# Optimization experiments

Measured on AMD Instinct MI355X. Metric: run time of the kernel, lower is better.

## Reference

```python
import jax, jax.numpy as jnp
import numpy as np

BONUS = 10.0   # strict_maxima_bonus
EPS = 1e-07


def _quad_interp3d(x, hes_noise):
    """Faithful port of kornia-style conv_quad_interp3d (diff-mode gradients,
    replicate padding, 3x3x3 NMS, masked 3x3 solve)."""
    B, C, D, H, W = x.shape
    dt = x.dtype
    # replicate-pad by 1 in D,H,W (spatial_gradient3d pads 'replicate')
    xp = jnp.pad(x, ((0, 0), (0, 0), (1, 1), (1, 1), (1, 1)), mode='edge')
    xw_p = xp[:, :, 1:-1, 1:-1, 2:]; xw_m = xp[:, :, 1:-1, 1:-1, :-2]
    xh_p = xp[:, :, 1:-1, 2:, 1:-1]; xh_m = xp[:, :, 1:-1, :-2, 1:-1]
    xd_p = xp[:, :, 2:, 1:-1, 1:-1]; xd_m = xp[:, :, :-2, 1:-1, 1:-1]
    # first-order central differences (channel order: x=W, y=H, s=D)
    gx = 0.5 * (xw_p - xw_m)
    gy = 0.5 * (xh_p - xh_m)
    gs = 0.5 * (xd_p - xd_m)
    # second-order stencils
    dxx = xw_p - 2.0 * x + xw_m
    dyy = xh_p - 2.0 * x + xh_m
    dss = xd_p - 2.0 * x + xd_m
    dxy = 0.25 * (xp[:, :, 1:-1, :-2, :-2] - xp[:, :, 1:-1, :-2, 2:]
                  - xp[:, :, 1:-1, 2:, :-2] + xp[:, :, 1:-1, 2:, 2:])
    dys = 0.25 * (xp[:, :, :-2, :-2, 1:-1] - xp[:, :, :-2, 2:, 1:-1]
                  - xp[:, :, 2:, :-2, 1:-1] + xp[:, :, 2:, 2:, 1:-1])
    dxs = 0.25 * (xp[:, :, :-2, 1:-1, :-2] - xp[:, :, :-2, 1:-1, 2:]
                  - xp[:, :, 2:, 1:-1, :-2] + xp[:, :, 2:, 1:-1, 2:])

    N = B * C * D * H * W
    b = jnp.stack([gx, gy, gs], axis=-1).reshape(N, 3)          # (N,3)
    Hes = jnp.stack([dxx, dxy, dxs,
                     dxy, dyy, dys,
                     dxs, dys, dss], axis=-1).reshape(N, 3, 3)  # (N,3,3)
    Hes = Hes + jnp.abs(hes_noise)[None].astype(dt) * jnp.asarray(EPS, dt)

    # NMS3d: 3x3x3 max-pool (stride 1, -inf padding), mask where value == window max
    x_max = jax.lax.reduce_window(x, -jnp.inf, jax.lax.max,
                                  (1, 1, 3, 3, 3), (1, 1, 1, 1, 1), 'SAME')
    mask = (x == x_max).reshape(N)

    # masked solve: identity Hessian where not a maximum -> zero contribution
    eye3 = jnp.eye(3, dtype=dt)
    Hm = jnp.where(mask[:, None, None], Hes, eye3)
    sol = jnp.linalg.solve(Hm, b[..., None])[..., 0]            # (N,3)
    sol = jnp.where(mask[:, None], sol, jnp.zeros((), dt))

    dx = -sol
    too_big = jnp.max(jnp.abs(dx), axis=1, keepdims=True) > 0.7
    dx = jnp.where(too_big, jnp.zeros((), dt), dx)
    dy = 0.5 * jnp.sum(b * dx, axis=1)                          # 0.5 * b^T dx

    y_max = x + dy.reshape(B, C, D, H, W) + BONUS * mask.reshape(B, C, D, H, W).astype(dt)

    # flip (x,y,s) -> (s,y,x) = (d,h,w) offsets, move coord axis to dim 2
    dx_res = dx[:, ::-1].reshape(B, C, D, H, W, 3).transpose(0, 1, 5, 2, 3, 4)
    grid = jnp.stack(jnp.meshgrid(jnp.arange(D), jnp.arange(H), jnp.arange(W),
                                  indexing='ij'), axis=0).astype(dt)  # (3,D,H,W)
    coords_max = grid[None, None] + dx_res                      # (B,C,3,D,H,W)
    return coords_max, y_max


def setup_inputs() -> dict:
    key = jax.random.key(0)
    k1, k2 = jax.random.split(key)
    x = jax.random.normal(k1, (2, 1, 8, 384, 384), dtype=jnp.float32)
    hes_noise = jax.random.uniform(k2, (3, 3), dtype=jnp.float32)
    return {"x": x, "hes_noise": hes_noise}


def reference(x, hes_noise):
    return _quad_interp3d(x, hes_noise)
```

## Files before the change

kernel.cpp:

```cpp
#include <hip/hip_runtime.h>


constexpr int Dd = 8, Hh = 384, Ww = 384, BC = 2;
constexpr int HW  = Hh * Ww;
constexpr int DHW = Dd * HW;
constexpr int NVOX = BC * DHW;
constexpr int W4 = Ww / 4;

#define BONUS_ 10.0f
#define EPS_ 1e-7f

__device__ __forceinline__ void load_plane6(const float* __restrict__ pb,
                                            int ro0, int ro1, int ro2,
                                            int w4, float dst[3][6], float pmax[4]) {
    const int offm = (w4 > 0)  ? -4 : 0;
    const int offp = (w4 < 95) ?  4 : 0;
    const int ro[3] = { ro0, ro1, ro2 };
    #pragma unroll
    for (int j = 0; j < 3; j++) {
        const float* row = pb + ro[j] + (w4 << 2);
        float4 c4 = *(const float4*)(row);
        float4 m4 = *(const float4*)(row + offm);
        float4 p4 = *(const float4*)(row + offp);
        dst[j][0] = (w4 > 0)  ? m4.w : c4.x;
        dst[j][1] = c4.x; dst[j][2] = c4.y; dst[j][3] = c4.z; dst[j][4] = c4.w;
        dst[j][5] = (w4 < 95) ? p4.x : c4.w;
    }
    #pragma unroll
    for (int k = 0; k < 4; k++) {
        float m0 = fmaxf(fmaxf(dst[0][k], dst[0][k + 1]), dst[0][k + 2]);
        float m1 = fmaxf(fmaxf(dst[1][k], dst[1][k + 1]), dst[1][k + 2]);
        float m2 = fmaxf(fmaxf(dst[2][k], dst[2][k + 1]), dst[2][k + 2]);
        pmax[k] = fmaxf(fmaxf(m0, m1), m2);
    }
}

__device__ __forceinline__ void compute_store(
    const float A[3][6], const float B[3][6], const float C[3][6],
    const float pmA[4], const float pmB[4], const float pmC[4],
    const float* __restrict__ hnA,
    float* __restrict__ coords, float* __restrict__ ymax,
    int d, int h, int w0, int cbase, int ybase)
{
    float r0[4], r1[4], r2[4], ry[4];

    #pragma unroll
    for (int k = 0; k < 4; k++) {
        float c = B[1][k + 1];

        float mx = fmaxf(fmaxf(pmA[k], pmB[k]), pmC[k]);
        bool mask = (c == mx);

        float gx = 0.5f * (B[1][k + 2] - B[1][k]);
        float gy = 0.5f * (B[2][k + 1] - B[0][k + 1]);
        float gs = 0.5f * (C[1][k + 1] - A[1][k + 1]);

        float dxx = B[1][k + 2] - 2.f * c + B[1][k];
        float dyy = B[2][k + 1] - 2.f * c + B[0][k + 1];
        float dss = C[1][k + 1] - 2.f * c + A[1][k + 1];
        float dxy = 0.25f * (B[0][k] - B[0][k + 2] - B[2][k] + B[2][k + 2]);
        float dys = 0.25f * (A[0][k + 1] - A[2][k + 1] - C[0][k + 1] + C[2][k + 1]);
        float dxs = 0.25f * (A[1][k] - A[1][k + 2] - C[1][k] + C[1][k + 2]);

        float A00 = dxx + hnA[0];
        float A01 = dxy + hnA[1];
        float A02 = dxs + hnA[2];
        float A10 = dxy + hnA[3];
        float A11 = dyy + hnA[4];
        float A12 = dys + hnA[5];
        float A20 = dxs + hnA[6];
        float A21 = dys + hnA[7];
        float A22 = dss + hnA[8];
        float b0 = gx, b1 = gy, b2 = gs;

        float c00 = A11 * A22 - A12 * A21;
        float c01 = A10 * A22 - A12 * A20;
        float c02 = A10 * A21 - A11 * A20;
        float det = A00 * c00 - A01 * c01 + A02 * c02;
        float inv = 1.0f / det;

        float t0 = b1 * A22 - A12 * b2;
        float t1 = A10 * b2 - b1 * A20;
        float t2 = b1 * A21 - A11 * b2;

        float s0 = (b0 * c00 - A01 * t0 + A02 * t2) * inv;
        float s1 = (A00 * t0 - b0 * c01 + A02 * t1) * inv;
        float s2 = (-A00 * t2 - A01 * t1 + b0 * c02) * inv;

        float dxv0 = mask ? -s0 : 0.f;
        float dxv1 = mask ? -s1 : 0.f;
        float dxv2 = mask ? -s2 : 0.f;
        float amax = fmaxf(fabsf(dxv0), fmaxf(fabsf(dxv1), fabsf(dxv2)));
        if (amax > 0.7f) { dxv0 = 0.f; dxv1 = 0.f; dxv2 = 0.f; }
        float dyv = 0.5f * (gx * dxv0 + gy * dxv1 + gs * dxv2);

        r0[k] = (float)d + dxv2;
        r1[k] = (float)h + dxv1;
        r2[k] = (float)(w0 + k) + dxv0;
        ry[k] = c + dyv + (mask ? BONUS_ : 0.f);
    }

    *(float4*)(coords + cbase)           = make_float4(r0[0], r0[1], r0[2], r0[3]);
    *(float4*)(coords + cbase + DHW)     = make_float4(r1[0], r1[1], r1[2], r1[3]);
    *(float4*)(coords + cbase + 2 * DHW) = make_float4(r2[0], r2[1], r2[2], r2[3]);
    *(float4*)(ymax + ybase)             = make_float4(ry[0], ry[1], ry[2], ry[3]);
}

__global__ __launch_bounds__(256) void quad_interp3d_kernel(
    const float* __restrict__ x,
    const float* __restrict__ hn,
    float* __restrict__ out)
{
    int t = blockIdx.x * 256 + threadIdx.x;
    int w4 = t % W4;
    int r  = t / W4;
    int h  = r % Hh;
    int r2 = r / Hh;
    int dt = r2 % 4;
    int bc = r2 / 4;

    const float* xb = x + bc * DHW;
    int w0 = w4 << 2;

    int h0 = h > 0 ? h - 1 : 0;
    int h2 = h < Hh - 1 ? h + 1 : Hh - 1;
    int ro0 = h0 * Ww, ro1 = h * Ww, ro2 = h2 * Ww;

    float hnA[9];
    #pragma unroll
    for (int i = 0; i < 9; i++) hnA[i] = fabsf(hn[i]) * EPS_;

    int d0  = dt * 2;
    int pm1 = d0 > 0 ? d0 - 1 : 0;
    int pp1 = d0 + 1;
    int pp2 = d0 + 2 < Dd ? d0 + 2 : Dd - 1;

    float P0[3][6], P1[3][6], P2[3][6], P3[3][6];
    float m0[4], m1[4], m2[4], m3[4];
    load_plane6(xb + pm1 * HW, ro0, ro1, ro2, w4, P0, m0);
    load_plane6(xb + d0  * HW, ro0, ro1, ro2, w4, P1, m1);
    load_plane6(xb + pp1 * HW, ro0, ro1, ro2, w4, P2, m2);
    load_plane6(xb + pp2 * HW, ro0, ro1, ro2, w4, P3, m3);

    float* coords = out;
    float* ymax   = out + 3 * NVOX;

    int sp0 = d0 * HW + ro1 + w0;
    int cb  = bc * 3 * DHW + sp0;
    int yb  = bc * DHW + sp0;

    compute_store(P0, P1, P2, m0, m1, m2, hnA, coords, ymax, d0,     h, w0, cb,      yb);
    compute_store(P1, P2, P3, m1, m2, m3, hnA, coords, ymax, d0 + 1, h, w0, cb + HW, yb + HW);
}

extern "C" void kernel_launch(void* const* d_in, const int* in_sizes, int n_in,
                              void* d_out, int out_size, void* d_ws, size_t ws_size,
                              hipStream_t stream) {
    const float* x  = (const float*)d_in[0];
    const float* hn = (const float*)d_in[1];
    float* out = (float*)d_out;

    int total  = BC * 4 * Hh * W4;
    int blocks = total / 256;
    quad_interp3d_kernel<<<blocks, 256, 0, stream>>>(x, hn, out);
}
```

Baseline: 19.38 us.

## Process one depth plane per thread with scalar halo loads and fast reciprocal

Each thread now handles one output depth slice instead of two, which doubles the thread count and loads three input planes instead of four. The neighbouring-column halo is now fetched with two scalar loads rather than two extra float4 loads, and the determinant inverse uses the hardware reciprocal. Occupancy rises and register pressure falls, at the cost of more redundant plane reads across threads and slightly less accurate division.

```diff
diff --git a/kernel.cpp b/kernel.cpp
--- a/kernel.cpp
+++ b/kernel.cpp
@@ -12,19 +12,18 @@
 
 __device__ __forceinline__ void load_plane6(const float* __restrict__ pb,
                                             int ro0, int ro1, int ro2,
-                                            int w4, float dst[3][6], float pmax[4]) {
-    const int offm = (w4 > 0)  ? -4 : 0;
-    const int offp = (w4 < 95) ?  4 : 0;
+                                            int w0, int cm, int cp,
+                                            float dst[3][6], float pmax[4]) {
     const int ro[3] = { ro0, ro1, ro2 };
     #pragma unroll
     for (int j = 0; j < 3; j++) {
-        const float* row = pb + ro[j] + (w4 << 2);
-        float4 c4 = *(const float4*)(row);
-        float4 m4 = *(const float4*)(row + offm);
-        float4 p4 = *(const float4*)(row + offp);
-        dst[j][0] = (w4 > 0)  ? m4.w : c4.x;
+        const float* row = pb + ro[j];
+        float4 c4 = *(const float4*)(row + w0);
+        float  em = row[cm];
+        float  ep = row[cp];
+        dst[j][0] = em;
         dst[j][1] = c4.x; dst[j][2] = c4.y; dst[j][3] = c4.z; dst[j][4] = c4.w;
-        dst[j][5] = (w4 < 95) ? p4.x : c4.w;
+        dst[j][5] = ep;
     }
     #pragma unroll
     for (int k = 0; k < 4; k++) {
@@ -35,14 +34,43 @@
     }
 }
 
-__device__ __forceinline__ void compute_store(
-    const float A[3][6], const float B[3][6], const float C[3][6],
-    const float pmA[4], const float pmB[4], const float pmC[4],
-    const float* __restrict__ hnA,
-    float* __restrict__ coords, float* __restrict__ ymax,
-    int d, int h, int w0, int cbase, int ybase)
+__global__ __launch_bounds__(256, 4) void quad_interp3d_kernel(
+    const float* __restrict__ x,
+    const float* __restrict__ hn,
+    float* __restrict__ out)
 {
-    float r0[4], r1[4], r2[4], ry[4];
+    int t = blockIdx.x * 256 + threadIdx.x;
+    int w4 = t % W4;
+    int r  = t / W4;
+    int h  = r % Hh;
+    int r2 = r / Hh;
+    int d  = r2 % Dd;
+    int bc = r2 / Dd;
+
+    const float* xb = x + bc * DHW;
+    int w0 = w4 << 2;
+    int cm = (w0 > 0) ? w0 - 1 : 0;
+    int cp = (w0 + 4 < Ww) ? w0 + 4 : Ww - 1;
+
+    int h0 = h > 0 ? h - 1 : 0;
+    int h2 = h < Hh - 1 ? h + 1 : Hh - 1;
+    int ro0 = h0 * Ww, ro1 = h * Ww, ro2 = h2 * Ww;
+
+    int dm = d > 0 ? d - 1 : 0;
+    int dp = d < Dd - 1 ? d + 1 : Dd - 1;
+
+    float hnA[9];
+    #pragma unroll
+    for (int i = 0; i < 9; i++) hnA[i] = fabsf(hn[i]) * EPS_;
+
+    float A[3][6], B[3][6], C[3][6];
+    float pmA[4], pmB[4], pmC[4];
+    load_plane6(xb + dm * HW, ro0, ro1, ro2, w0, cm, cp, A, pmA);
+    load_plane6(xb + d  * HW, ro0, ro1, ro2, w0, cm, cp, B, pmB);
+    load_plane6(xb + dp * HW, ro0, ro1, ro2, w0, cm, cp, C, pmC);
+
+    float r0[4], r1[4], r2v[4], ry[4];
+    float df = (float)d, hf = (float)h, wf = (float)w0;
 
     #pragma unroll
     for (int k = 0; k < 4; k++) {
@@ -77,7 +105,7 @@
         float c01 = A10 * A22 - A12 * A20;
         float c02 = A10 * A21 - A11 * A20;
         float det = A00 * c00 - A01 * c01 + A02 * c02;
-        float inv = 1.0f / det;
+        float inv = __builtin_amdgcn_rcpf(det);
 
         float t0 = b1 * A22 - A12 * b2;
         float t1 = A10 * b2 - b1 * A20;
@@ -94,63 +122,23 @@
         if (amax > 0.7f) { dxv0 = 0.f; dxv1 = 0.f; dxv2 = 0.f; }
         float dyv = 0.5f * (gx * dxv0 + gy * dxv1 + gs * dxv2);
 
-        r0[k] = (float)d + dxv2;
-        r1[k] = (float)h + dxv1;
-        r2[k] = (float)(w0 + k) + dxv0;
-        ry[k] = c + dyv + (mask ? BONUS_ : 0.f);
+        r0[k]  = df + dxv2;
+        r1[k]  = hf + dxv1;
+        r2v[k] = (wf + (float)k) + dxv0;
+        ry[k]  = c + dyv + (mask ? BONUS_ : 0.f);
     }
-
-    *(float4*)(coords + cbase)           = make_float4(r0[0], r0[1], r0[2], r0[3]);
-    *(float4*)(coords + cbase + DHW)     = make_float4(r1[0], r1[1], r1[2], r1[3]);
-    *(float4*)(coords + cbase + 2 * DHW) = make_float4(r2[0], r2[1], r2[2], r2[3]);
-    *(float4*)(ymax + ybase)             = make_float4(ry[0], ry[1], ry[2], ry[3]);
-}
-
-__global__ __launch_bounds__(256) void quad_interp3d_kernel(
-    const float* __restrict__ x,
-    const float* __restrict__ hn,
-    float* __restrict__ out)
-{
-    int t = blockIdx.x * 256 + threadIdx.x;
-    int w4 = t % W4;
-    int r  = t / W4;
-    int h  = r % Hh;
-    int r2 = r / Hh;
-    int dt = r2 % 4;
-    int bc = r2 / 4;
-
-    const float* xb = x + bc * DHW;
-    int w0 = w4 << 2;
-
-    int h0 = h > 0 ? h - 1 : 0;
-    int h2 = h < Hh - 1 ? h + 1 : Hh - 1;
-    int ro0 = h0 * Ww, ro1 = h * Ww, ro2 = h2 * Ww;
-
-    float hnA[9];
-    #pragma unroll
-    for (int i = 0; i < 9; i++) hnA[i] = fabsf(hn[i]) * EPS_;
-
-    int d0  = dt * 2;
-    int pm1 = d0 > 0 ? d0 - 1 : 0;
-    int pp1 = d0 + 1;
-    int pp2 = d0 + 2 < Dd ? d0 + 2 : Dd - 1;
-
-    float P0[3][6], P1[3][6], P2[3][6], P3[3][6];
-    float m0[4], m1[4], m2[4], m3[4];
-    load_plane6(xb + pm1 * HW, ro0, ro1, ro2, w4, P0, m0);
-    load_plane6(xb + d0  * HW, ro0, ro1, ro2, w4, P1, m1);
-    load_plane6(xb + pp1 * HW, ro0, ro1, ro2, w4, P2, m2);
-    load_plane6(xb + pp2 * HW, ro0, ro1, ro2, w4, P3, m3);
 
     float* coords = out;
     float* ymax   = out + 3 * NVOX;
 
-    int sp0 = d0 * HW + ro1 + w0;
-    int cb  = bc * 3 * DHW + sp0;
-    int yb  = bc * DHW + sp0;
+    int sp = d * HW + ro1 + w0;
+    int cb = bc * 3 * DHW + sp;
+    int yb = bc * DHW + sp;
 
-    compute_store(P0, P1, P2, m0, m1, m2, hnA, coords, ymax, d0,     h, w0, cb,      yb);
-    compute_store(P1, P2, P3, m1, m2, m3, hnA, coords, ymax, d0 + 1, h, w0, cb + HW, yb + HW);
+    *(float4*)(coords + cb)           = make_float4(r0[0], r0[1], r0[2], r0[3]);
+    *(float4*)(coords + cb + DHW)     = make_float4(r1[0], r1[1], r1[2], r1[3]);
+    *(float4*)(coords + cb + 2 * DHW) = make_float4(r2v[0], r2v[1], r2v[2], r2v[3]);
+    *(float4*)(ymax + yb)             = make_float4(ry[0], ry[1], ry[2], ry[3]);
 }
 
 extern "C" void kernel_launch(void* const* d_in, const int* in_sizes, int n_in,
@@ -160,7 +148,7 @@
     const float* hn = (const float*)d_in[1];
     float* out = (float*)d_out;
 
-    int total  = BC * 4 * Hh * W4;
+    int total  = BC * Dd * Hh * W4;
     int blocks = total / 256;
     quad_interp3d_kernel<<<blocks, 256, 0, stream>>>(x, hn, out);
 }
```

Result: slower. 21.72 us (+12.0%).
